# Kernel optimization log

Measured on AMD Instinct MI355X. Metric: run time of the kernel, lower is better.

The kernel has to match this reference:

```python
import jax, jax.numpy as jnp
import numpy as np
from jax import lax

B, D, E, H, W = 256, 64, 16, 64, 64
PROJ, FC, NA = 512, 1024, 2

def _conv(x, w, pad):
    # x: [N,C,H,W], w: [O,I,kh,kw]
    return lax.conv_general_dilated(x, w, (1, 1), [(pad, pad), (pad, pad)],
                                    dimension_numbers=('NCHW', 'OIHW', 'NCHW'))

def _maxpool2(x):
    return lax.reduce_window(x, -jnp.inf, lax.max, (1, 1, 2, 2), (1, 1, 2, 2), 'VALID')

def _sample_conv(x, w, b):
    # per-sample conv with its own gathered expert weights: x [D,h,w], w [D,D,3,3]
    y = lax.conv_general_dilated(x[None], w, (1, 1), [(1, 1), (1, 1)],
                                 dimension_numbers=('NCHW', 'OIHW', 'NCHW'))[0]
    return y + b[:, None, None]

_expert_conv = jax.vmap(_sample_conv)  # batch of samples, each with its own kernel

def setup_inputs() -> dict:
    key = jax.random.key(0)
    ks = jax.random.split(key, 12)
    s = 0.05
    return {
        'image': jax.random.normal(ks[0], (B, 3, H, W), jnp.float32),
        'question': jax.random.randint(ks[1], (B, 8), 0, E),
        'stem_w0': jax.random.normal(ks[2], (D, 3, 3, 3), jnp.float32) * s,
        'stem_b0': jnp.zeros((D,), jnp.float32),
        'stem_w': jax.random.normal(ks[3], (3, D, D, 3, 3), jnp.float32) * s,
        'stem_b': jnp.zeros((3, D), jnp.float32),
        'exp_w1': jax.random.normal(ks[4], (E, D, D, 3, 3), jnp.float32) * s,
        'exp_b1': jnp.zeros((E, D), jnp.float32),
        'exp_w2': jax.random.normal(ks[5], (E, D, D, 3, 3), jnp.float32) * s,
        'exp_b2': jnp.zeros((E, D), jnp.float32),
        'proj_w': jax.random.normal(ks[6], (PROJ, D, 1, 1), jnp.float32) * s,
        'proj_b': jnp.zeros((PROJ,), jnp.float32),
        'fc1_w': jax.random.normal(ks[7], (FC, PROJ * 8 * 8), jnp.float32) * 0.01,
        'fc1_b': jnp.zeros((FC,), jnp.float32),
        'fc2_w': jax.random.normal(ks[8], (NA, FC), jnp.float32) * 0.01,
        'fc2_b': jnp.zeros((NA,), jnp.float32),
    }

def reference(image, question, stem_w0, stem_b0, stem_w, stem_b,
              exp_w1, exp_b1, exp_w2, exp_b2,
              proj_w, proj_b, fc1_w, fc1_b, fc2_w, fc2_b):
    # --- stem: 4 conv3x3 + ReLU, maxpool after layers 0 and 2 (64->32->16) ---
    h = jax.nn.relu(_conv(image, stem_w0, 1) + stem_b0[None, :, None, None])
    h = _maxpool2(h)
    h = jax.nn.relu(_conv(h, stem_w[0], 1) + stem_b[0][None, :, None, None])
    h = jax.nn.relu(_conv(h, stem_w[1], 1) + stem_b[1][None, :, None, None])
    h = _maxpool2(h)
    h = jax.nn.relu(_conv(h, stem_w[2], 1) + stem_b[2][None, :, None, None])
    # --- chain1 routing: cols (lhs=4, rel=5, rhs=7) each pick a ResidualBlock expert ---
    for col in (4, 5, 7):
        idx = question[:, col]                       # [B] expert ids
        w1, b1 = exp_w1[idx], exp_b1[idx]            # gather per-sample kernels
        w2, b2 = exp_w2[idx], exp_b2[idx]
        mid = jax.nn.relu(_expert_conv(h, w1, b1))   # conv1 + ReLU
        out = _expert_conv(mid, w2, b2)              # conv2 (no BN)
        h = jax.nn.relu(h + out)                     # residual + ReLU
    # --- classifier: 1x1 proj + ReLU, maxpool2, flatten, fc, fc ---
    c = jax.nn.relu(_conv(h, proj_w, 0) + proj_b[None, :, None, None])  # [B,512,16,16]
    c = _maxpool2(c)                                                     # [B,512,8,8]
    c = c.reshape(c.shape[0], -1)                                        # [B,32768]
    c = jax.nn.relu(c @ fc1_w.T + fc1_b)
    return c @ fc2_w.T + fc2_b                                           # [B,2]
```

## Files before the change

### kernel.cpp

```cpp
#include <hip/hip_runtime.h>
#include <cstddef>


typedef _Float16 half8 __attribute__((ext_vector_type(8)));
typedef _Float16 half4_t __attribute__((ext_vector_type(4)));
typedef float f32x4 __attribute__((ext_vector_type(4)));

#define LO_SCALE 2048.0f
#define LO_INV (1.0f / 2048.0f)

__global__ void transw_k(const float* __restrict__ src, float* __restrict__ dst,
                         int O, int I, int K, int total) {
    int id = blockIdx.x * 256 + threadIdx.x;
    if (id >= total) return;
    int OIK = O * I * K;
    int n = id / OIK, rem = id % OIK;
    int o = rem / (I * K), r2 = rem % (I * K);
    int i = r2 / K, k = r2 % K;
    dst[(size_t)n * OIK + (i * K + k) * O + o] = src[id];
}

__global__ void wxform_k(const float* __restrict__ src, _Float16* __restrict__ dst,
                         int nlayers) {
    int id = blockIdx.x * 256 + threadIdx.x;
    if (id >= nlayers * 36864) return;
    int layer = id / 36864, idx = id % 36864;
    int j = idx & 7, l = (idx >> 3) & 63, nt = (idx >> 9) & 3;
    int icc = (idx >> 11) & 1, tap = idx >> 12;
    int kl = (l >> 4) * 8 + j, ic = icc * 32 + kl, oc = nt * 16 + (l & 15);
    float v = src[(size_t)layer * 36864 + (oc * 64 + ic) * 9 + tap];
    _Float16 hi = (_Float16)v;
    _Float16 lo = (_Float16)((v - (float)hi) * LO_SCALE);
    dst[(size_t)layer * 73728 + idx] = hi;
    dst[(size_t)layer * 73728 + 36864 + idx] = lo;
}

__global__ void pwxform_k(const float* __restrict__ src, _Float16* __restrict__ dst) {
    int id = blockIdx.x * 256 + threadIdx.x;
    if (id >= 32768) return;
    int j = id & 7, l = (id >> 3) & 63, icc = (id >> 9) & 1, nt = id >> 10;
    int kl = (l >> 4) * 8 + j, ic = icc * 32 + kl, oc = nt * 16 + (l & 15);
    float v = src[oc * 64 + ic];
    _Float16 hi = (_Float16)v;
    _Float16 lo = (_Float16)((v - (float)hi) * LO_SCALE);
    dst[id] = hi;
    dst[32768 + id] = lo;
}

__global__ __launch_bounds__(256, 4)
void conv1_k(const float* __restrict__ img, const float* __restrict__ w0t,
             const float* __restrict__ b0, _Float16* __restrict__ out) {
    const size_t NE1 = 16777216;
    int b = blockIdx.x, tile = blockIdx.y, ocg = blockIdx.z;
    int typ = (tile >> 1) * 16, txp = (tile & 1) * 16;
    int cy0 = typ * 2, cx0 = txp * 2;
    __shared__ float lds[3][34][34];
    const float* imb = img + (size_t)b * 3 * 64 * 64;
    for (int i = threadIdx.x; i < 3 * 34 * 34; i += 256) {
        int c = i / 1156, rem = i % 1156, r = rem / 34, cc = rem % 34;
        int gy = cy0 - 1 + r, gx = cx0 - 1 + cc;
        float v = 0.f;
        if (gy >= 0 && gy < 64 && gx >= 0 && gx < 64) v = imb[(c * 64 + gy) * 64 + gx];
        lds[c][r][cc] = v;
    }
    __syncthreads();
    int pyl = threadIdx.x >> 4, pxl = threadIdx.x & 15;
    float win[3][4][4];
#pragma unroll
    for (int c = 0; c < 3; ++c)
#pragma unroll
        for (int wy = 0; wy < 4; ++wy)
#pragma unroll
            for (int wx = 0; wx < 4; ++wx)
                win[c][wy][wx] = lds[c][2 * pyl + wy][2 * pxl + wx];
    int py = typ + pyl, px = txp + pxl;
    size_t obase = (((size_t)b * 32 + py) * 32 + px) * 64;
#pragma unroll
    for (int q = 0; q < 4; ++q) {
        int ocq = ocg * 4 + q;
        float acc[4][4] = {};
#pragma unroll
        for (int c = 0; c < 3; ++c)
#pragma unroll
            for (int ky = 0; ky < 3; ++ky)
#pragma unroll
                for (int kx = 0; kx < 3; ++kx) {
                    float4 w = *(const float4*)&w0t[(c * 9 + ky * 3 + kx) * 64 + ocq * 4];
                    float wv4[4] = {w.x, w.y, w.z, w.w};
#pragma unroll
                    for (int p2 = 0; p2 < 4; ++p2) {
                        float iv = win[c][(p2 >> 1) + ky][(p2 & 1) + kx];
#pragma unroll
                        for (int o = 0; o < 4; ++o)
                            acc[p2][o] = fmaf(iv, wv4[o], acc[p2][o]);
                    }
                }
        half4_t rh, rl;
#pragma unroll
        for (int o = 0; o < 4; ++o) {
            float bvv = b0[ocq * 4 + o];
            float m = fmaxf(fmaxf(acc[0][o], acc[1][o]), fmaxf(acc[2][o], acc[3][o]));
            float v = fmaxf(m + bvv, 0.f);
            _Float16 h = (_Float16)v;
            rh[o] = h;
            rl[o] = (_Float16)((v - (float)h) * LO_SCALE);
        }
        *(half4_t*)&out[obase + ocq * 4] = rh;
        *(half4_t*)&out[NE1 + obase + ocq * 4] = rl;
    }
}

template <int S, bool POOL, bool RES>
__global__ __launch_bounds__(256, 2)
void convm_k(const _Float16* __restrict__ in, _Float16* __restrict__ out,
             const _Float16* __restrict__ wf, const float* __restrict__ bias,
             const _Float16* __restrict__ res, const int* __restrict__ question,
             int qcol) {
    constexpr size_t NEin = (size_t)S * S * 64 * 256;
    constexpr size_t NEout = POOL ? NEin / 4 : NEin;
    int b = blockIdx.x, t = blockIdx.y;
    constexpr int NTX = S / 16;
    int ty0 = (t / NTX) * 8, tx0 = (t % NTX) * 16;

    __shared__ __align__(16) _Float16 lds[2 * 7200];

    int tid = threadIdx.x, lane = tid & 63, wv = tid >> 6;
    const _Float16* wb = wf;
    const float* bb = bias;
    if (question) {
        int idx = question[b * 8 + qcol];
        wb += (size_t)idx * 73728;
        bb += idx * 64;
    }
    float bv[4];
#pragma unroll
    for (int nt = 0; nt < 4; ++nt) bv[nt] = bb[nt * 16 + (lane & 15)];

    f32x4 acc1[2][4] = {};
    f32x4 acc2[2][4] = {};

    int am = lane & 15;
    int k0 = (lane >> 4) * 8;

    for (int icc = 0; icc < 2; ++icc) {
        __syncthreads();
        for (int i = tid; i < 720; i += 256) {
            int pix = i >> 2, j8 = (i & 3) * 8;
            int hy = pix / 18, hx = pix % 18;
            int gy = ty0 + hy - 1, gx = tx0 + hx - 1;
            half8 vh = {}, vl = {};
            if (gy >= 0 && gy < S && gx >= 0 && gx < S) {
                size_t src = (((size_t)b * S + gy) * S + gx) * 64 + icc * 32 + j8;
                vh = *(const half8*)&in[src];
                vl = *(const half8*)&in[NEin + src];
            }
            *(half8*)&lds[pix * 40 + j8] = vh;
            *(half8*)&lds[7200 + pix * 40 + j8] = vl;
        }
        __syncthreads();

#pragma unroll
        for (int ky = 0; ky < 3; ++ky)
#pragma unroll
            for (int kx = 0; kx < 3; ++kx) {
                int tap = ky * 3 + kx;
                const _Float16* wp = wb + (tap * 2 + icc) * 2048 + lane * 8;
                half8 bhi[4], blo[4];
#pragma unroll
                for (int nt = 0; nt < 4; ++nt) {
                    bhi[nt] = *(const half8*)(wp + nt * 512);
                    blo[nt] = *(const half8*)(wp + nt * 512 + 36864);
                }
#pragma unroll
                for (int mt = 0; mt < 2; ++mt) {
                    int MT = wv * 2 + mt;
                    int Q = MT * 4 + (am >> 2), s = am & 3;
                    int py = (Q >> 3) * 2 + (s >> 1), px = (Q & 7) * 2 + (s & 1);
                    const _Float16* ap = &lds[((py + ky) * 18 + (px + kx)) * 40 + k0];
                    half8 ahi = *(const half8*)ap;
                    half8 alo = *(const half8*)(ap + 7200);
#pragma unroll
                    for (int nt = 0; nt < 4; ++nt) {
                        acc1[mt][nt] = __builtin_amdgcn_mfma_f32_16x16x32_f16(
                            ahi, bhi[nt], acc1[mt][nt], 0, 0, 0);
                        acc2[mt][nt] = __builtin_amdgcn_mfma_f32_16x16x32_f16(
                            ahi, blo[nt], acc2[mt][nt], 0, 0, 0);
                        acc2[mt][nt] = __builtin_amdgcn_mfma_f32_16x16x32_f16(
                            alo, bhi[nt], acc2[mt][nt], 0, 0, 0);
                    }
                }
            }
    }

    int cn = lane & 15, rq = lane >> 4;
#pragma unroll
    for (int mt = 0; mt < 2; ++mt) {
        int MT = wv * 2 + mt;
        int Q = MT * 4 + rq;
        int qy = Q >> 3, qx = Q & 7;
#pragma unroll
        for (int nt = 0; nt < 4; ++nt) {
            int oc = nt * 16 + cn;
            float vals[4];
#pragma unroll
            for (int r = 0; r < 4; ++r)
                vals[r] = acc1[mt][nt][r] + acc2[mt][nt][r] * LO_INV + bv[nt];
            if (POOL) {
                float m = fmaxf(fmaxf(vals[0], vals[1]), fmaxf(vals[2], vals[3]));
                m = fmaxf(m, 0.f);
                int opy = (ty0 >> 1) + qy, opx = (tx0 >> 1) + qx;
                size_t o = (((size_t)b * (S / 2) + opy) * (S / 2) + opx) * 64 + oc;
                _Float16 h = (_Float16)m;
                out[o] = h;
                out[NEout + o] = (_Float16)((m - (float)h) * LO_SCALE);
            } else {
#pragma unroll
                for (int r = 0; r < 4; ++r) {
                    int py = qy * 2 + (r >> 1), px = qx * 2 + (r & 1);
                    size_t o = (((size_t)b * S + (ty0 + py)) * S + (tx0 + px)) * 64 + oc;
                    float v = vals[r];
                    if (RES) v += (float)res[o] + (float)res[NEin + o] * LO_INV;
                    v = fmaxf(v, 0.f);
                    _Float16 h = (_Float16)v;
                    out[o] = h;
                    out[NEout + o] = (_Float16)((v - (float)h) * LO_SCALE);
                }
            }
        }
    }
}

__global__ __launch_bounds__(256)
void projm_k(const _Float16* __restrict__ in ,
             const _Float16* __restrict__ pw, const float* __restrict__ bias,
             _Float16* __restrict__ outh ) {
    const size_t NE2 = 4194304;
    int b = blockIdx.x;
    __shared__ float lt[64 * 65];
    int tid = threadIdx.x, lane = tid & 63, wv = tid >> 6;
    int row = lane & 15, cseg = lane >> 4;

    half8 ah[4][2], al[4][2];
#pragma unroll
    for (int mt = 0; mt < 4; ++mt) {
        int MT = wv * 4 + mt;
        int Q = MT * 4 + (row >> 2), s = row & 3;
        int y = (Q >> 3) * 2 + (s >> 1), x = (Q & 7) * 2 + (s & 1);
        size_t pb = ((size_t)b * 256 + y * 16 + x) * 64 + cseg * 8;
#pragma unroll
        for (int icc = 0; icc < 2; ++icc) {
            ah[mt][icc] = *(const half8*)&in[pb + icc * 32];
            al[mt][icc] = *(const half8*)&in[NE2 + pb + icc * 32];
        }
    }

    for (int ogl = 0; ogl < 4; ++ogl) {
        int og = blockIdx.y * 4 + ogl;
        half8 bh[4][2], bl[4][2];
#pragma unroll
        for (int ntl = 0; ntl < 4; ++ntl)
#pragma unroll
            for (int icc = 0; icc < 2; ++icc) {
                int nt = og * 4 + ntl;
                const _Float16* wp = pw + ((nt * 2 + icc) * 64 + lane) * 8;
                bh[ntl][icc] = *(const half8*)wp;
                bl[ntl][icc] = *(const half8*)(wp + 32768);
            }
        f32x4 a1[4][4] = {};
        f32x4 a2[4][4] = {};
#pragma unroll
        for (int icc = 0; icc < 2; ++icc)
#pragma unroll
            for (int mt = 0; mt < 4; ++mt)
#pragma unroll
                for (int ntl = 0; ntl < 4; ++ntl) {
                    a1[mt][ntl] = __builtin_amdgcn_mfma_f32_16x16x32_f16(
                        ah[mt][icc], bh[ntl][icc], a1[mt][ntl], 0, 0, 0);
                    a2[mt][ntl] = __builtin_amdgcn_mfma_f32_16x16x32_f16(
                        ah[mt][icc], bl[ntl][icc], a2[mt][ntl], 0, 0, 0);
                    a2[mt][ntl] = __builtin_amdgcn_mfma_f32_16x16x32_f16(
                        al[mt][icc], bh[ntl][icc], a2[mt][ntl], 0, 0, 0);
                }
        if (ogl) __syncthreads();
#pragma unroll
        for (int mt = 0; mt < 4; ++mt) {
            int Qg = (wv * 4 + mt) * 4 + (lane >> 4);
#pragma unroll
            for (int ntl = 0; ntl < 4; ++ntl) {
                float bvv = bias[og * 64 + ntl * 16 + (lane & 15)];
                float v0 = a1[mt][ntl][0] + a2[mt][ntl][0] * LO_INV + bvv;
                float v1 = a1[mt][ntl][1] + a2[mt][ntl][1] * LO_INV + bvv;
                float v2 = a1[mt][ntl][2] + a2[mt][ntl][2] * LO_INV + bvv;
                float v3 = a1[mt][ntl][3] + a2[mt][ntl][3] * LO_INV + bvv;
                float m = fmaxf(fmaxf(fmaxf(v0, v1), fmaxf(v2, v3)), 0.f);
                lt[(ntl * 16 + (lane & 15)) * 65 + Qg] = m;
            }
        }
        __syncthreads();
#pragma unroll
        for (int r = 0; r < 16; ++r) {
            int f = r * 256 + tid;
            int ol = f >> 6, q = f & 63;
            float v = lt[ol * 65 + q];
            _Float16 h = (_Float16)v;
            _Float16 l = (_Float16)((v - (float)h) * LO_SCALE);
            size_t o = (size_t)b * 32768 + og * 4096 + ol * 64 + q;
            outh[o] = h;
            outh[8388608 + o] = l;
        }
    }
}

__global__ __launch_bounds__(256)
void fc1m_k(const _Float16* __restrict__ Ahl ,
            const float* __restrict__ W,
            float* __restrict__ partial ) {
    int bid = blockIdx.x;
    int lid = (bid & 7) * 64 + (bid >> 3);
    int mt = lid & 1, nt = (lid >> 1) & 7, ks = lid >> 4;
    int m0 = mt * 128, n0 = nt * 128;
    const _Float16* Ab = Ahl + (size_t)m0 * 32768 + ks * 1024;
    const float* Wb = W + (size_t)n0 * 32768 + ks * 1024;

    __shared__ __align__(16) _Float16 lds[40960];

    int tid = threadIdx.x, lane = tid & 63, wv = tid >> 6;
    int wm = (wv & 1) * 64, wn = (wv >> 1) * 64;
    int koff = (lane >> 4) * 8, fr = lane & 15;

    f32x4 acc1[4][4] = {};
    f32x4 acc2[4][4] = {};

    int arow[2], ak8[2];
#pragma unroll
    for (int p = 0; p < 2; ++p) {
        int idx = p * 256 + tid;
        arow[p] = idx >> 2;
        ak8[p] = (idx & 3) * 8;
    }
    int wrow[4], wc4[4];
#pragma unroll
    for (int p = 0; p < 4; ++p) {
        int idx = p * 256 + tid;
        wrow[p] = idx >> 3;
        wc4[p] = (idx & 7) << 2;
    }

    half8 pa_h[2], pa_l[2];
    float4 rw[4];

#pragma unroll
    for (int p = 0; p < 2; ++p) {
        pa_h[p] = *(const half8*)&Ab[(size_t)arow[p] * 32768 + ak8[p]];
        pa_l[p] = *(const half8*)&Ab[8388608 + (size_t)arow[p] * 32768 + ak8[p]];
    }
#pragma unroll
    for (int p = 0; p < 4; ++p)
        rw[p] = *(const float4*)&Wb[(size_t)wrow[p] * 32768 + wc4[p]];
    {
        _Float16* b0p = lds;
#pragma unroll
        for (int p = 0; p < 2; ++p) {
            *(half8*)&b0p[arow[p] * 40 + ak8[p]] = pa_h[p];
            *(half8*)&b0p[5120 + arow[p] * 40 + ak8[p]] = pa_l[p];
        }
#pragma unroll
        for (int p = 0; p < 4; ++p) {
            float4 u = rw[p];
            _Float16 g0 = (_Float16)u.x, g1 = (_Float16)u.y;
            _Float16 g2 = (_Float16)u.z, g3 = (_Float16)u.w;
            half4_t gh = {g0, g1, g2, g3};
            half4_t gl = {(_Float16)((u.x - (float)g0) * LO_SCALE),
                          (_Float16)((u.y - (float)g1) * LO_SCALE),
                          (_Float16)((u.z - (float)g2) * LO_SCALE),
                          (_Float16)((u.w - (float)g3) * LO_SCALE)};
            *(half4_t*)&b0p[10240 + wrow[p] * 40 + wc4[p]] = gh;
            *(half4_t*)&b0p[15360 + wrow[p] * 40 + wc4[p]] = gl;
        }
    }
#pragma unroll
    for (int p = 0; p < 2; ++p) {
        pa_h[p] = *(const half8*)&Ab[(size_t)arow[p] * 32768 + 32 + ak8[p]];
        pa_l[p] = *(const half8*)&Ab[8388608 + (size_t)arow[p] * 32768 + 32 + ak8[p]];
    }
#pragma unroll
    for (int p = 0; p < 4; ++p)
        rw[p] = *(const float4*)&Wb[(size_t)wrow[p] * 32768 + 32 + wc4[p]];
    __syncthreads();

    for (int kt = 0; kt < 32; ++kt) {
        _Float16* cur = lds + (kt & 1) * 20480;
        _Float16* nxt = lds + ((kt + 1) & 1) * 20480;
        if (kt < 31) {
#pragma unroll
            for (int p = 0; p < 2; ++p) {
                *(half8*)&nxt[arow[p] * 40 + ak8[p]] = pa_h[p];
                *(half8*)&nxt[5120 + arow[p] * 40 + ak8[p]] = pa_l[p];
            }
#pragma unroll
            for (int p = 0; p < 4; ++p) {
                float4 u = rw[p];
                _Float16 g0 = (_Float16)u.x, g1 = (_Float16)u.y;
                _Float16 g2 = (_Float16)u.z, g3 = (_Float16)u.w;
                half4_t gh = {g0, g1, g2, g3};
                half4_t gl = {(_Float16)((u.x - (float)g0) * LO_SCALE),
                              (_Float16)((u.y - (float)g1) * LO_SCALE),
                              (_Float16)((u.z - (float)g2) * LO_SCALE),
                              (_Float16)((u.w - (float)g3) * LO_SCALE)};
                *(half4_t*)&nxt[10240 + wrow[p] * 40 + wc4[p]] = gh;
                *(half4_t*)&nxt[15360 + wrow[p] * 40 + wc4[p]] = gl;
            }
            if (kt < 30) {
                int kb = (kt + 2) * 32;
#pragma unroll
                for (int p = 0; p < 2; ++p) {
                    pa_h[p] = *(const half8*)&Ab[(size_t)arow[p] * 32768 + kb + ak8[p]];
                    pa_l[p] = *(const half8*)&Ab[8388608 + (size_t)arow[p] * 32768 + kb + ak8[p]];
                }
#pragma unroll
                for (int p = 0; p < 4; ++p)
                    rw[p] = *(const float4*)&Wb[(size_t)wrow[p] * 32768 + kb + wc4[p]];
            }
        }
        half8 bh[4], bl[4];
#pragma unroll
        for (int nf = 0; nf < 4; ++nf) {
            int r = wn + nf * 16 + fr;
            bh[nf] = *(const half8*)&cur[10240 + r * 40 + koff];
            bl[nf] = *(const half8*)&cur[15360 + r * 40 + koff];
        }
#pragma unroll
        for (int mf = 0; mf < 4; ++mf) {
            int r = wm + mf * 16 + fr;
            half8 ah = *(const half8*)&cur[r * 40 + koff];
            half8 al = *(const half8*)&cur[5120 + r * 40 + koff];
#pragma unroll
            for (int nf = 0; nf < 4; ++nf) {
                acc1[mf][nf] = __builtin_amdgcn_mfma_f32_16x16x32_f16(
                    ah, bh[nf], acc1[mf][nf], 0, 0, 0);
                acc2[mf][nf] = __builtin_amdgcn_mfma_f32_16x16x32_f16(
                    ah, bl[nf], acc2[mf][nf], 0, 0, 0);
                acc2[mf][nf] = __builtin_amdgcn_mfma_f32_16x16x32_f16(
                    al, bh[nf], acc2[mf][nf], 0, 0, 0);
            }
        }
        __syncthreads();
    }

    int rq = lane >> 4, cn = lane & 15;
    float* pb = partial + (size_t)ks * 262144;
#pragma unroll
    for (int mf = 0; mf < 4; ++mf)
#pragma unroll
        for (int nf = 0; nf < 4; ++nf) {
            int n = n0 + wn + nf * 16 + cn;
#pragma unroll
            for (int r = 0; r < 4; ++r) {
                int m = m0 + wm + mf * 16 + rq * 4 + r;
                pb[(size_t)m * 1024 + n] = acc1[mf][nf][r] + acc2[mf][nf][r] * LO_INV;
            }
        }
}

__global__ __launch_bounds__(256)
void fc1red_k(const float* __restrict__ partial, const float* __restrict__ b1,
              float* __restrict__ fc1o_t ) {
    int m = blockIdx.x;
    int n0 = threadIdx.x * 4;
    float4 s = {0.f, 0.f, 0.f, 0.f};
    for (int ks = 0; ks < 32; ++ks) {
        float4 v = *(const float4*)&partial[((size_t)ks * 256 + m) * 1024 + n0];
        s.x += v.x; s.y += v.y; s.z += v.z; s.w += v.w;
    }
    fc1o_t[(size_t)(n0 + 0) * 256 + m] = fmaxf(s.x + b1[n0 + 0], 0.f);
    fc1o_t[(size_t)(n0 + 1) * 256 + m] = fmaxf(s.y + b1[n0 + 1], 0.f);
    fc1o_t[(size_t)(n0 + 2) * 256 + m] = fmaxf(s.z + b1[n0 + 2], 0.f);
    fc1o_t[(size_t)(n0 + 3) * 256 + m] = fmaxf(s.w + b1[n0 + 3], 0.f);
}

__global__ __launch_bounds__(256)
void fc2a_k(const float* __restrict__ a_t, const float* __restrict__ W2,
            float* __restrict__ p2) {
    int n2 = blockIdx.x, ks = blockIdx.y;
    int m = threadIdx.x;
    float acc = 0.f;
    for (int k = ks * 256; k < ks * 256 + 256; ++k)
        acc = fmaf(a_t[(size_t)k * 256 + m], W2[n2 * 1024 + k], acc);
    p2[((size_t)n2 * 4 + ks) * 256 + m] = acc;
}

__global__ __launch_bounds__(512)
void fc2b_k(const float* __restrict__ p2, const float* __restrict__ b2,
            float* __restrict__ out) {
    int i = threadIdx.x;
    int m = i >> 1, n2 = i & 1;
    float s = b2[n2];
#pragma unroll
    for (int ks = 0; ks < 4; ++ks) s += p2[((size_t)n2 * 4 + ks) * 256 + m];
    out[m * 2 + n2] = s;
}

extern "C" void kernel_launch(void* const* d_in, const int* in_sizes, int n_in,
                              void* d_out, int out_size, void* d_ws, size_t ws_size,
                              hipStream_t stream) {
    const float* image   = (const float*)d_in[0];
    const int*   question= (const int*)d_in[1];
    const float* stem_w0 = (const float*)d_in[2];
    const float* stem_b0 = (const float*)d_in[3];
    const float* stem_w  = (const float*)d_in[4];
    const float* stem_b  = (const float*)d_in[5];
    const float* exp_w1  = (const float*)d_in[6];
    const float* exp_b1  = (const float*)d_in[7];
    const float* exp_w2  = (const float*)d_in[8];
    const float* exp_b2  = (const float*)d_in[9];
    const float* proj_w  = (const float*)d_in[10];
    const float* proj_b  = (const float*)d_in[11];
    const float* fc1_w   = (const float*)d_in[12];
    const float* fc1_b   = (const float*)d_in[13];
    const float* fc2_w   = (const float*)d_in[14];
    const float* fc2_b   = (const float*)d_in[15];
    (void)in_sizes; (void)n_in; (void)out_size; (void)ws_size;

    float* ws = (float*)d_ws;
    const size_t A = 16777216, P2N = 4194304;
    float* wtr   = ws + 2 * A + P2N;
    float* w0t   = wtr;
    _Float16* pwF = (_Float16*)(wtr + 1728);
    float* pfc2  = wtr + 1728 + 32768;
    _Float16* f16b = (_Float16*)(wtr + 36544);
    _Float16* stemtF = f16b;
    _Float16* e1tF   = f16b + 3 * 73728;
    _Float16* e2tF   = e1tF + 16 * 73728;
    _Float16* p1h  = (_Float16*)ws;
    _Float16* h2h  = (_Float16*)(ws + A);
    _Float16* p2h  = (_Float16*)(ws + 2 * A);
    _Float16* hAh  = (_Float16*)ws;
    _Float16* hBh  = (_Float16*)(ws + P2N);
    _Float16* hCh  = (_Float16*)(ws + 2 * P2N);
    _Float16* pool3h = (_Float16*)(ws + A);
    float* fc1o  = ws + A + 8388608;
    float* fc1p  = ws;

    transw_k<<<(1728 + 255) / 256, 256, 0, stream>>>(stem_w0, w0t, 64, 3, 9, 1728);
    pwxform_k<<<128, 256, 0, stream>>>(proj_w, pwF);
    wxform_k<<<(3 * 36864 + 255) / 256, 256, 0, stream>>>(stem_w, stemtF, 3);
    wxform_k<<<(16 * 36864 + 255) / 256, 256, 0, stream>>>(exp_w1, e1tF, 16);
    wxform_k<<<(16 * 36864 + 255) / 256, 256, 0, stream>>>(exp_w2, e2tF, 16);

    conv1_k<<<dim3(256, 4, 4), 256, 0, stream>>>(image, w0t, stem_b0, p1h);
    convm_k<32, false, false><<<dim3(256, 8), 256, 0, stream>>>(
        p1h, h2h, stemtF, stem_b, nullptr, nullptr, 0);
    convm_k<32, true, false><<<dim3(256, 8), 256, 0, stream>>>(
        h2h, p2h, stemtF + 73728, stem_b + 64, nullptr, nullptr, 0);
    convm_k<16, false, false><<<dim3(256, 2), 256, 0, stream>>>(
        p2h, hAh, stemtF + 2 * 73728, stem_b + 128, nullptr, nullptr, 0);

    const int cols[3] = {4, 5, 7};
    _Float16* hin = hAh;
    _Float16* hmid = hBh;
    _Float16* hout = hCh;
    for (int r = 0; r < 3; ++r) {
        convm_k<16, false, false><<<dim3(256, 2), 256, 0, stream>>>(
            hin, hmid, e1tF, exp_b1, nullptr, question, cols[r]);
        convm_k<16, false, true><<<dim3(256, 2), 256, 0, stream>>>(
            hmid, hout, e2tF, exp_b2, hin, question, cols[r]);
        _Float16* tp = hin; hin = hout; hout = hmid; hmid = tp;
    }

    projm_k<<<dim3(256, 2), 256, 0, stream>>>(hin, pwF, proj_b, pool3h);
    fc1m_k<<<512, 256, 0, stream>>>(pool3h, fc1_w, fc1p);
    fc1red_k<<<256, 256, 0, stream>>>(fc1p, fc1_b, fc1o);
    fc2a_k<<<dim3(2, 4), 256, 0, stream>>>(fc1o, fc2_w, pfc2);
    fc2b_k<<<1, 512, 0, stream>>>(pfc2, fc2_b, (float*)d_out);
}
```

Before: 464.3 us.

## Rewrite first stem conv as im2col MFMA GEMM with split-fp16 precision

```diff
diff --git a/kernel.cpp b/kernel.cpp
--- a/kernel.cpp
+++ b/kernel.cpp
@@ -8,17 +8,6 @@
 
 #define LO_SCALE 2048.0f
 #define LO_INV (1.0f / 2048.0f)
-
-__global__ void transw_k(const float* __restrict__ src, float* __restrict__ dst,
-                         int O, int I, int K, int total) {
-    int id = blockIdx.x * 256 + threadIdx.x;
-    if (id >= total) return;
-    int OIK = O * I * K;
-    int n = id / OIK, rem = id % OIK;
-    int o = rem / (I * K), r2 = rem % (I * K);
-    int i = r2 / K, k = r2 % K;
-    dst[(size_t)n * OIK + (i * K + k) * O + o] = src[id];
-}
 
 __global__ void wxform_k(const float* __restrict__ src, _Float16* __restrict__ dst,
                          int nlayers) {
@@ -47,66 +36,117 @@
     dst[32768 + id] = lo;
 }
 
-__global__ __launch_bounds__(256, 4)
-void conv1_k(const float* __restrict__ img, const float* __restrict__ w0t,
-             const float* __restrict__ b0, _Float16* __restrict__ out) {
+__global__ void c1wx_k(const float* __restrict__ src, _Float16* __restrict__ dst) {
+    int id = blockIdx.x * 256 + threadIdx.x;
+    if (id >= 2048) return;
+    int j = id & 7, l = (id >> 3) & 63, nt = id >> 9;
+    int k = (l >> 4) * 8 + j, oc = nt * 16 + (l & 15);
+    float v = 0.f;
+    if (k < 27) {
+        int ic = k / 9, tap = k % 9;
+        v = src[(oc * 3 + ic) * 9 + tap];
+    }
+    _Float16 hi = (_Float16)v;
+    _Float16 lo = (_Float16)((v - (float)hi) * LO_SCALE);
+    dst[id] = hi;
+    dst[2048 + id] = lo;
+}
+
+__global__ __launch_bounds__(256, 2)
+void conv1m_k(const float* __restrict__ img, const _Float16* __restrict__ wf,
+              const float* __restrict__ b0, _Float16* __restrict__ out) {
     const size_t NE1 = 16777216;
-    int b = blockIdx.x, tile = blockIdx.y, ocg = blockIdx.z;
-    int typ = (tile >> 1) * 16, txp = (tile & 1) * 16;
-    int cy0 = typ * 2, cx0 = txp * 2;
-    __shared__ float lds[3][34][34];
+    int b = blockIdx.x, t = blockIdx.y;
+    int ty0 = (t >> 2) * 8, tx0 = (t & 3) * 16;
+    __shared__ float halo[3][10][18];
+    __shared__ __align__(16) _Float16 lin[2 * 5120];
+
+    int tid = threadIdx.x, lane = tid & 63, wv = tid >> 6;
     const float* imb = img + (size_t)b * 3 * 64 * 64;
-    for (int i = threadIdx.x; i < 3 * 34 * 34; i += 256) {
-        int c = i / 1156, rem = i % 1156, r = rem / 34, cc = rem % 34;
-        int gy = cy0 - 1 + r, gx = cx0 - 1 + cc;
+    for (int i = tid; i < 540; i += 256) {
+        int c = i / 180, rem = i % 180, r = rem / 18, cc = rem % 18;
+        int gy = ty0 - 1 + r, gx = tx0 - 1 + cc;
         float v = 0.f;
         if (gy >= 0 && gy < 64 && gx >= 0 && gx < 64) v = imb[(c * 64 + gy) * 64 + gx];
-        lds[c][r][cc] = v;
+        halo[c][r][cc] = v;
     }
     __syncthreads();
-    int pyl = threadIdx.x >> 4, pxl = threadIdx.x & 15;
-    float win[3][4][4];
-#pragma unroll
-    for (int c = 0; c < 3; ++c)
-#pragma unroll
-        for (int wy = 0; wy < 4; ++wy)
-#pragma unroll
-            for (int wx = 0; wx < 4; ++wx)
-                win[c][wy][wx] = lds[c][2 * pyl + wy][2 * pxl + wx];
-    int py = typ + pyl, px = txp + pxl;
-    size_t obase = (((size_t)b * 32 + py) * 32 + px) * 64;
-#pragma unroll
-    for (int q = 0; q < 4; ++q) {
-        int ocq = ocg * 4 + q;
-        float acc[4][4] = {};
-#pragma unroll
-        for (int c = 0; c < 3; ++c)
-#pragma unroll
-            for (int ky = 0; ky < 3; ++ky)
-#pragma unroll
-                for (int kx = 0; kx < 3; ++kx) {
-                    float4 w = *(const float4*)&w0t[(c * 9 + ky * 3 + kx) * 64 + ocq * 4];
-                    float wv4[4] = {w.x, w.y, w.z, w.w};
-#pragma unroll
-                    for (int p2 = 0; p2 < 4; ++p2) {
-                        float iv = win[c][(p2 >> 1) + ky][(p2 & 1) + kx];
-#pragma unroll
-                        for (int o = 0; o < 4; ++o)
-                            acc[p2][o] = fmaf(iv, wv4[o], acc[p2][o]);
-                    }
-                }
-        half4_t rh, rl;
-#pragma unroll
-        for (int o = 0; o < 4; ++o) {
-            float bvv = b0[ocq * 4 + o];
-            float m = fmaxf(fmaxf(acc[0][o], acc[1][o]), fmaxf(acc[2][o], acc[3][o]));
-            float v = fmaxf(m + bvv, 0.f);
+    for (int i = tid; i < 512; i += 256) {
+        int r = i >> 2, j8 = (i & 3) * 8;
+        int MT = r >> 4, am = r & 15;
+        int Q = MT * 4 + (am >> 2), s = am & 3;
+        int py = (Q >> 3) * 2 + (s >> 1), px = (Q & 7) * 2 + (s & 1);
+        half8 vh, vl;
+#pragma unroll
+        for (int j = 0; j < 8; ++j) {
+            int k = j8 + j;
+            float v = 0.f;
+            if (k < 27) {
+                int ic = k / 9, tap = k % 9;
+                v = halo[ic][py + tap / 3][px + tap % 3];
+            }
             _Float16 h = (_Float16)v;
-            rh[o] = h;
-            rl[o] = (_Float16)((v - (float)h) * LO_SCALE);
-        }
-        *(half4_t*)&out[obase + ocq * 4] = rh;
-        *(half4_t*)&out[NE1 + obase + ocq * 4] = rl;
+            vh[j] = h;
+            vl[j] = (_Float16)((v - (float)h) * LO_SCALE);
+        }
+        *(half8*)&lin[r * 40 + j8] = vh;
+        *(half8*)&lin[5120 + r * 40 + j8] = vl;
+    }
+    __syncthreads();
+
+    int am = lane & 15, k0 = (lane >> 4) * 8;
+    float bv[4];
+#pragma unroll
+    for (int nt = 0; nt < 4; ++nt) bv[nt] = b0[nt * 16 + (lane & 15)];
+
+    half8 bh[4], bl[4];
+#pragma unroll
+    for (int nt = 0; nt < 4; ++nt) {
+        const _Float16* wp = wf + ((size_t)nt * 64 + lane) * 8;
+        bh[nt] = *(const half8*)wp;
+        bl[nt] = *(const half8*)(wp + 2048);
+    }
+
+    f32x4 acc1[2][4] = {};
+    f32x4 acc2[2][4] = {};
+#pragma unroll
+    for (int mt = 0; mt < 2; ++mt) {
+        int MT = wv * 2 + mt;
+        const _Float16* ap = &lin[(MT * 16 + am) * 40 + k0];
+        half8 ahi = *(const half8*)ap;
+        half8 alo = *(const half8*)(ap + 5120);
+#pragma unroll
+        for (int nt = 0; nt < 4; ++nt) {
+            acc1[mt][nt] = __builtin_amdgcn_mfma_f32_16x16x32_f16(
+                ahi, bh[nt], acc1[mt][nt], 0, 0, 0);
+            acc2[mt][nt] = __builtin_amdgcn_mfma_f32_16x16x32_f16(
+                ahi, bl[nt], acc2[mt][nt], 0, 0, 0);
+            acc2[mt][nt] = __builtin_amdgcn_mfma_f32_16x16x32_f16(
+                alo, bh[nt], acc2[mt][nt], 0, 0, 0);
+        }
+    }
+
+    int cn = lane & 15, rq = lane >> 4;
+#pragma unroll
+    for (int mt = 0; mt < 2; ++mt) {
+        int MT = wv * 2 + mt;
+        int Q = MT * 4 + rq;
+        int qy = Q >> 3, qx = Q & 7;
+#pragma unroll
+        for (int nt = 0; nt < 4; ++nt) {
+            int oc = nt * 16 + cn;
+            float vals[4];
+#pragma unroll
+            for (int r = 0; r < 4; ++r)
+                vals[r] = acc1[mt][nt][r] + acc2[mt][nt][r] * LO_INV + bv[nt];
+            float m = fmaxf(fmaxf(vals[0], vals[1]), fmaxf(vals[2], vals[3]));
+            m = fmaxf(m, 0.f);
+            int opy = (ty0 >> 1) + qy, opx = (tx0 >> 1) + qx;
+            size_t o = (((size_t)b * 32 + opy) * 32 + opx) * 64 + oc;
+            _Float16 h = (_Float16)m;
+            out[o] = h;
+            out[NE1 + o] = (_Float16)((m - (float)h) * LO_SCALE);
+        }
     }
 }
 
@@ -524,10 +564,10 @@
     float* ws = (float*)d_ws;
     const size_t A = 16777216, P2N = 4194304;
     float* wtr   = ws + 2 * A + P2N;
-    float* w0t   = wtr;
-    _Float16* pwF = (_Float16*)(wtr + 1728);
-    float* pfc2  = wtr + 1728 + 32768;
-    _Float16* f16b = (_Float16*)(wtr + 36544);
+    _Float16* c1wF = (_Float16*)wtr;
+    _Float16* pwF = (_Float16*)(wtr + 2048);
+    float* pfc2  = wtr + 2048 + 32768;
+    _Float16* f16b = (_Float16*)(wtr + 36864);
     _Float16* stemtF = f16b;
     _Float16* e1tF   = f16b + 3 * 73728;
     _Float16* e2tF   = e1tF + 16 * 73728;
@@ -541,13 +581,13 @@
     float* fc1o  = ws + A + 8388608;
     float* fc1p  = ws;
 
-    transw_k<<<(1728 + 255) / 256, 256, 0, stream>>>(stem_w0, w0t, 64, 3, 9, 1728);
+    c1wx_k<<<8, 256, 0, stream>>>(stem_w0, c1wF);
     pwxform_k<<<128, 256, 0, stream>>>(proj_w, pwF);
     wxform_k<<<(3 * 36864 + 255) / 256, 256, 0, stream>>>(stem_w, stemtF, 3);
     wxform_k<<<(16 * 36864 + 255) / 256, 256, 0, stream>>>(exp_w1, e1tF, 16);
     wxform_k<<<(16 * 36864 + 255) / 256, 256, 0, stream>>>(exp_w2, e2tF, 16);
 
-    conv1_k<<<dim3(256, 4, 4), 256, 0, stream>>>(image, w0t, stem_b0, p1h);
+    conv1m_k<<<dim3(256, 32), 256, 0, stream>>>(image, c1wF, stem_b0, p1h);
     convm_k<32, false, false><<<dim3(256, 8), 256, 0, stream>>>(
         p1h, h2h, stemtF, stem_b, nullptr, nullptr, 0);
     convm_k<32, true, false><<<dim3(256, 8), 256, 0, stream>>>(
```

Result: faster. 437.1 us, median of 3 (-5.9%).
